# Performance work log

Hardware: AMD Instinct MI355X
Metric: run time of the kernel (lower is better)

Reference implementation:

```python
import jax, jax.numpy as jnp
import numpy as np

SRC_V, TRG_V = 36616, 23262
EMB, ENC_H, DEC_H = 300, 512, 1024
S, T, B = 50, 50, 128


def setup_inputs() -> dict:
    key = jax.random.key(0)
    ks = jax.random.split(key, 17)
    sc = 0.05
    n = lambda k, shp: (jax.random.normal(k, shp, jnp.float32) * sc)
    return {
        "input_src_batch": jax.random.randint(ks[0], (S, B), 0, SRC_V),
        "input_trg_batch": jax.random.randint(ks[1], (T, B), 0, TRG_V),
        "EEMB": n(ks[2], (SRC_V, EMB)),
        "enc_Wih_f": n(ks[3], (4 * ENC_H, EMB)),
        "enc_Whh_f": n(ks[4], (4 * ENC_H, ENC_H)),
        "enc_b_f": n(ks[5], (4 * ENC_H,)),
        "enc_Wih_r": n(ks[6], (4 * ENC_H, EMB)),
        "enc_Whh_r": n(ks[7], (4 * ENC_H, ENC_H)),
        "enc_b_r": n(ks[8], (4 * ENC_H,)),
        "attn_Wi": n(ks[9], (DEC_H, DEC_H)),
        "attn_Wo": n(ks[10], (DEC_H, 2 * DEC_H)),
        "dec_Wih": n(ks[11], (4 * DEC_H, DEC_H + EMB)),
        "dec_Whh": n(ks[12], (4 * DEC_H, DEC_H)),
        "dec_b": n(ks[13], (4 * DEC_H,)),
        "DEMB": n(ks[14], (TRG_V, EMB)),
        "gen_W": n(ks[15], (TRG_V, DEC_H)),
        "gen_b": n(ks[16], (TRG_V,)),
    }


def lstm_step(h, c, x, Wih, Whh, b):
    # PyTorch gate order: i, f, g, o
    g = x @ Wih.T + h @ Whh.T + b
    i, f, gg, o = jnp.split(g, 4, axis=-1)
    c2 = jax.nn.sigmoid(f) * c + jax.nn.sigmoid(i) * jnp.tanh(gg)
    h2 = jax.nn.sigmoid(o) * jnp.tanh(c2)
    return h2, c2


def reference(input_src_batch, input_trg_batch, EEMB, enc_Wih_f, enc_Whh_f,
              enc_b_f, enc_Wih_r, enc_Whh_r, enc_b_r, attn_Wi, attn_Wo,
              dec_Wih, dec_Whh, dec_b, DEMB, gen_W, gen_b):
    batch = input_src_batch.shape[1]
    sent_len = input_trg_batch.shape[0]
    emb = EEMB[input_src_batch]  # [S, B, 300]

    def scan_dir(xs, Wih, Whh, b):
        def f(carry, x):
            h, c = carry
            h2, c2 = lstm_step(h, c, x, Wih, Whh, b)
            return (h2, c2), h2
        init = (jnp.zeros((batch, ENC_H), emb.dtype),
                jnp.zeros((batch, ENC_H), emb.dtype))
        (hF, cF), hs = jax.lax.scan(f, init, xs)
        return hs, hF, cF

    hs_f, hF, cF = scan_dir(emb, enc_Wih_f, enc_Whh_f, enc_b_f)
    hs_r, hR, cR = scan_dir(emb[::-1], enc_Wih_r, enc_Whh_r, enc_b_r)
    hs_r = hs_r[::-1]
    enc_out = jnp.concatenate([hs_f, hs_r], axis=-1)  # [S, B, 1024]
    # torch permute(1,2,0).view(B,1024) interleaves fwd/rev per feature
    hidden = jnp.stack([hF, hR], axis=-1).reshape(batch, DEC_H)
    context = jnp.stack([cF, cR], axis=-1).reshape(batch, DEC_H)

    def attn(h):
        semi = h @ attn_Wi.T                                # [B,1024]
        score = jnp.einsum('sbd,bd->sb', enc_out, semi)     # [S,B]
        alpha = jax.nn.softmax(score, axis=0)               # softmax over src len
        s_tilde = jnp.einsum('sb,sbd->bd', alpha, enc_out)  # [B,1024]
        return jnp.tanh(jnp.concatenate([s_tilde, h], axis=1) @ attn_Wo.T)

    trg_emb = DEMB[input_trg_batch[: sent_len - 1]]  # [T-1, B, 300]

    def step(carry, x_emb):
        h, c = carry
        c_t = attn(h)
        dec_in = jnp.concatenate([c_t, x_emb], axis=1)  # [B, 1324]
        h2, c2 = lstm_step(h, c, dec_in, dec_Wih, dec_Whh, dec_b)
        logp = jax.nn.log_softmax(h2 @ gen_W.T + gen_b, axis=1)
        return (h2, c2), logp

    _, outs = jax.lax.scan(step, (hidden, context), trg_emb)  # [T-1,B,V]
    out0 = jnp.zeros((1, batch, TRG_V), outs.dtype)
    return jnp.concatenate([out0, outs], axis=0)  # [T, B, V]
```

## Files before the change

### kernel.cpp

```cpp
#include <hip/hip_runtime.h>
#include <hip/hip_bf16.h>

#define S_LEN 50
#define T_LEN 50
#define BATCH 128
#define EMB 300
#define ENC_H 512
#define DEC_H 1024
#define TRG_V 23262
#define DEC_IN (DEC_H + EMB)
#define KCAT (DEC_IN + DEC_H)

static inline int cdiv(int a, int b) { return (a + b - 1) / b; }

__device__ __forceinline__ float sigm(float x) { return 1.f / (1.f + expf(-x)); }

typedef __attribute__((ext_vector_type(8))) short bf16x8;
typedef __attribute__((ext_vector_type(4))) float f32x4;

__device__ __forceinline__ void gload_lds16(const void* g, void* l) {
    __builtin_amdgcn_global_load_lds((const __attribute__((address_space(1))) int*)g,
                                     (__attribute__((address_space(3))) int*)l, 16, 0, 0);
}

__global__ __launch_bounds__(256)
void gemm_mfma_bf16(const __hip_bfloat16* __restrict__ A, const __hip_bfloat16* __restrict__ W,
                    const float* __restrict__ bias, float* __restrict__ C,
                    int M, int N, int K, int ldc)
{
    __shared__ short As[128 * 32];
    __shared__ short Bs[128 * 32];
    const int tid  = threadIdx.x;
    const int wave = tid >> 6;
    const int lane = tid & 63;
    const int m0 = blockIdx.y * 128;
    const int n0 = blockIdx.x * 128;
    const int wr = wave >> 1, wc = wave & 1;

    const int srow = lane >> 2;
    const int kgrp = lane & 3;
    const int arow0 = 32 * wave;

    f32x4 acc[4][4] = {};

    for (int k0 = 0; k0 < K; k0 += 32) {
#pragma unroll
        for (int c = 0; c < 2; c++) {
            int row = arow0 + 16 * c + srow;
            gload_lds16(A + (size_t)(m0 + row) * K + k0 + kgrp * 8,
                        &As[(arow0 + 16 * c) * 32]);
        }
#pragma unroll
        for (int c = 0; c < 2; c++) {
            int row = arow0 + 16 * c + srow;
            int gr = n0 + row; if (gr > N - 1) gr = N - 1;
            gload_lds16(W + (size_t)gr * K + k0 + kgrp * 8,
                        &Bs[(arow0 + 16 * c) * 32]);
        }
        __syncthreads();

        bf16x8 a[4], b[4];
#pragma unroll
        for (int mi = 0; mi < 4; mi++)
            a[mi] = *(const bf16x8*)&As[(wr * 64 + mi * 16 + (lane & 15)) * 32 + (lane >> 4) * 8];
#pragma unroll
        for (int ni = 0; ni < 4; ni++)
            b[ni] = *(const bf16x8*)&Bs[(wc * 64 + ni * 16 + (lane & 15)) * 32 + (lane >> 4) * 8];
#pragma unroll
        for (int mi = 0; mi < 4; mi++)
#pragma unroll
            for (int ni = 0; ni < 4; ni++)
                acc[mi][ni] = __builtin_amdgcn_mfma_f32_16x16x32_bf16(a[mi], b[ni], acc[mi][ni], 0, 0, 0);
        __syncthreads();
    }

#pragma unroll
    for (int mi = 0; mi < 4; mi++)
#pragma unroll
        for (int ni = 0; ni < 4; ni++) {
            int col = n0 + wc * 64 + ni * 16 + (lane & 15);
            if (col >= N) continue;
            float bv = bias[col];
#pragma unroll
            for (int r = 0; r < 4; r++) {
                int row = m0 + wr * 64 + mi * 16 + (lane >> 4) * 4 + r;
                C[(size_t)row * ldc + col] = acc[mi][ni][r] + bv;
            }
        }
}

__global__ void cast_f32_bf16(const float* __restrict__ in, __hip_bfloat16* __restrict__ out, size_t n)
{
    size_t i = ((size_t)blockIdx.x * blockDim.x + threadIdx.x) * 4;
    if (i + 3 < n) {
        float4 v = *(const float4*)(in + i);
        out[i + 0] = __float2bfloat16(v.x);
        out[i + 1] = __float2bfloat16(v.y);
        out[i + 2] = __float2bfloat16(v.z);
        out[i + 3] = __float2bfloat16(v.w);
    } else {
        for (; i < n; i++) out[i] = __float2bfloat16(in[i]);
    }
}

template<int BM, int BN, int BK, int TM, int TN, bool HAS_BIAS>
__global__ __launch_bounds__((BM / TM) * (BN / TN))
void gemm_bt(const float* __restrict__ A, const float* __restrict__ W,
             const float* __restrict__ bias, float* __restrict__ C,
             int M, int N, int K, int ldc)
{
    constexpr int NT  = (BM / TM) * (BN / TN);
    constexpr int NGA = TM / 4;
    constexpr int NGB = TN / 4;
    constexpr int GS  = (BN / TN) * 4;
    constexpr int LPA = BM * BK / 4 / NT;
    constexpr int LPB = BN * BK / 4 / NT;

    __shared__ float As[BK][BM + 4];
    __shared__ float Bs[BK][BN + 4];

    const int tid = threadIdx.x;
    const int tx = tid % (BN / TN);
    const int ty = tid / (BN / TN);
    const int m0 = blockIdx.y * BM;
    const int n0 = blockIdx.x * BN;

    float acc[TM][TN];
#pragma unroll
    for (int i = 0; i < TM; i++)
#pragma unroll
        for (int j = 0; j < TN; j++) acc[i][j] = 0.f;

    for (int k0 = 0; k0 < K; k0 += BK) {
#pragma unroll
        for (int e = 0; e < LPA; e++) {
            int idx = tid + e * NT;
            int r = idx / (BK / 4);
            int c4 = idx % (BK / 4);
            int row = m0 + r; if (row > M - 1) row = M - 1;
            int kk = k0 + c4 * 4;
            float4 v;
            if (kk + 3 < K) {
                v = *(const float4*)(A + (size_t)row * K + kk);
            } else {
                v.x = (kk + 0 < K) ? A[(size_t)row * K + kk + 0] : 0.f;
                v.y = (kk + 1 < K) ? A[(size_t)row * K + kk + 1] : 0.f;
                v.z = (kk + 2 < K) ? A[(size_t)row * K + kk + 2] : 0.f;
                v.w = (kk + 3 < K) ? A[(size_t)row * K + kk + 3] : 0.f;
            }
            As[c4 * 4 + 0][r] = v.x; As[c4 * 4 + 1][r] = v.y;
            As[c4 * 4 + 2][r] = v.z; As[c4 * 4 + 3][r] = v.w;
        }
#pragma unroll
        for (int e = 0; e < LPB; e++) {
            int idx = tid + e * NT;
            int r = idx / (BK / 4);
            int c4 = idx % (BK / 4);
            int row = n0 + r; if (row > N - 1) row = N - 1;
            int kk = k0 + c4 * 4;
            float4 v;
            if (kk + 3 < K) {
                v = *(const float4*)(W + (size_t)row * K + kk);
            } else {
                v.x = (kk + 0 < K) ? W[(size_t)row * K + kk + 0] : 0.f;
                v.y = (kk + 1 < K) ? W[(size_t)row * K + kk + 1] : 0.f;
                v.z = (kk + 2 < K) ? W[(size_t)row * K + kk + 2] : 0.f;
                v.w = (kk + 3 < K) ? W[(size_t)row * K + kk + 3] : 0.f;
            }
            Bs[c4 * 4 + 0][r] = v.x; Bs[c4 * 4 + 1][r] = v.y;
            Bs[c4 * 4 + 2][r] = v.z; Bs[c4 * 4 + 3][r] = v.w;
        }
        __syncthreads();
#pragma unroll
        for (int kk = 0; kk < BK; kk++) {
            float a[TM], b[TN];
#pragma unroll
            for (int g = 0; g < NGA; g++) {
                float4 v = *(const float4*)(&As[kk][ty * TM + g * 4]);
                a[g * 4 + 0] = v.x; a[g * 4 + 1] = v.y; a[g * 4 + 2] = v.z; a[g * 4 + 3] = v.w;
            }
#pragma unroll
            for (int g = 0; g < NGB; g++) {
                float4 v = *(const float4*)(&Bs[kk][tx * 4 + g * GS]);
                b[g * 4 + 0] = v.x; b[g * 4 + 1] = v.y; b[g * 4 + 2] = v.z; b[g * 4 + 3] = v.w;
            }
#pragma unroll
            for (int i = 0; i < TM; i++)
#pragma unroll
                for (int j = 0; j < TN; j++)
                    acc[i][j] = fmaf(a[i], b[j], acc[i][j]);
        }
        __syncthreads();
    }

#pragma unroll
    for (int i = 0; i < TM; i++) {
        int row = m0 + ty * TM + i;
        if (row >= M) continue;
#pragma unroll
        for (int g = 0; g < NGB; g++) {
            int colb = n0 + tx * 4 + g * GS;
#pragma unroll
            for (int j = 0; j < 4; j++) {
                int cc = colb + j;
                if (cc >= N) continue;
                float v = acc[i][g * 4 + j];
                if (HAS_BIAS) v += bias[cc];
                C[(size_t)row * ldc + cc] = v;
            }
        }
    }
}

struct StepArgs {
    const float* bias;
    const float* D0; const float* D1;
    float* cst0; float* cst1;
    float* hst0; float* hst1;
    float* enc_out;
    float* catA;
    float* attn_cat;
    float* cdec;
    __hip_bfloat16* H_bf;
    int t;
};

__device__ __forceinline__ float4 g4k(const float* base, int kk, int K) {
    float4 v = make_float4(0.f, 0.f, 0.f, 0.f);
    if (kk + 3 < K) v = *(const float4*)(base + kk);
    else {
        if (kk     < K) v.x = base[kk];
        if (kk + 1 < K) v.y = base[kk + 1];
        if (kk + 2 < K) v.z = base[kk + 2];
    }
    return v;
}

template<int EPI, bool DUAL>
__global__ __launch_bounds__(256)
void step_gemm(const float* __restrict__ A, const float* __restrict__ W, int K,
               const float* __restrict__ A1, const float* __restrict__ W1,
               StepArgs ea)
{
    __shared__ float As[2][32][36];
    __shared__ float Bs[2][32][68];
    const int tid = threadIdx.x;
    const int tx = tid & 15, ty = tid >> 4;
    const int m0 = blockIdx.y * 32, n0 = blockIdx.x * 64;
    const int dir = DUAL ? blockIdx.z : 0;
    const float* Ap = (DUAL && dir) ? A1 : A;
    const float* Wp = (DUAL && dir) ? W1 : W;

    const int ar = tid >> 3, ac4 = tid & 7;
    const float* abase  = Ap + (size_t)(m0 + ar) * K;
    const float* bbase0 = Wp + (size_t)(n0 + ar) * K;
    const float* bbase1 = bbase0 + (size_t)32 * K;

    float acc[2][4] = {{0.f,0.f,0.f,0.f},{0.f,0.f,0.f,0.f}};
    const int NIT = (K + 31) / 32;

    float4 pa, pb0, pb1;
    {
        int kk = ac4 * 4;
        if (32 <= K) { pa = *(const float4*)(abase + kk); pb0 = *(const float4*)(bbase0 + kk); pb1 = *(const float4*)(bbase1 + kk); }
        else { pa = g4k(abase, kk, K); pb0 = g4k(bbase0, kk, K); pb1 = g4k(bbase1, kk, K); }
    }
    *(float4*)&As[0][ar][ac4 * 4] = pa;
    Bs[0][ac4*4+0][ar]    = pb0.x; Bs[0][ac4*4+1][ar]    = pb0.y;
    Bs[0][ac4*4+2][ar]    = pb0.z; Bs[0][ac4*4+3][ar]    = pb0.w;
    Bs[0][ac4*4+0][ar+32] = pb1.x; Bs[0][ac4*4+1][ar+32] = pb1.y;
    Bs[0][ac4*4+2][ar+32] = pb1.z; Bs[0][ac4*4+3][ar+32] = pb1.w;
    __syncthreads();

    int cur = 0;
    for (int it = 0; it < NIT; ++it) {
        float4 qa, qb0, qb1;
        const bool has = (it + 1 < NIT);
        if (has) {
            int k0 = (it + 1) * 32;
            int kk = k0 + ac4 * 4;
            if (k0 + 32 <= K) { qa = *(const float4*)(abase + kk); qb0 = *(const float4*)(bbase0 + kk); qb1 = *(const float4*)(bbase1 + kk); }
            else { qa = g4k(abase, kk, K); qb0 = g4k(bbase0, kk, K); qb1 = g4k(bbase1, kk, K); }
        }
#pragma unroll
        for (int k4 = 0; k4 < 8; ++k4) {
            float4 a0 = *(const float4*)&As[cur][ty*2+0][k4*4];
            float4 a1 = *(const float4*)&As[cur][ty*2+1][k4*4];
            float4 b0 = *(const float4*)&Bs[cur][k4*4+0][tx*4];
            float4 b1 = *(const float4*)&Bs[cur][k4*4+1][tx*4];
            float4 b2 = *(const float4*)&Bs[cur][k4*4+2][tx*4];
            float4 b3 = *(const float4*)&Bs[cur][k4*4+3][tx*4];
            float av0[4] = {a0.x, a0.y, a0.z, a0.w};
            float av1[4] = {a1.x, a1.y, a1.z, a1.w};
            float4 bq[4] = {b0, b1, b2, b3};
#pragma unroll
            for (int q = 0; q < 4; q++) {
                acc[0][0] = fmaf(av0[q], bq[q].x, acc[0][0]);
                acc[0][1] = fmaf(av0[q], bq[q].y, acc[0][1]);
                acc[0][2] = fmaf(av0[q], bq[q].z, acc[0][2]);
                acc[0][3] = fmaf(av0[q], bq[q].w, acc[0][3]);
                acc[1][0] = fmaf(av1[q], bq[q].x, acc[1][0]);
                acc[1][1] = fmaf(av1[q], bq[q].y, acc[1][1]);
                acc[1][2] = fmaf(av1[q], bq[q].z, acc[1][2]);
                acc[1][3] = fmaf(av1[q], bq[q].w, acc[1][3]);
            }
        }
        if (has) {
            int nb = cur ^ 1;
            *(float4*)&As[nb][ar][ac4 * 4] = qa;
            Bs[nb][ac4*4+0][ar]    = qb0.x; Bs[nb][ac4*4+1][ar]    = qb0.y;
            Bs[nb][ac4*4+2][ar]    = qb0.z; Bs[nb][ac4*4+3][ar]    = qb0.w;
            Bs[nb][ac4*4+0][ar+32] = qb1.x; Bs[nb][ac4*4+1][ar+32] = qb1.y;
            Bs[nb][ac4*4+2][ar+32] = qb1.z; Bs[nb][ac4*4+3][ar+32] = qb1.w;
        }
        __syncthreads();
        cur ^= 1;
    }

    const int cb = n0 + tx * 4;
    if (EPI == 1) {
#pragma unroll
        for (int i = 0; i < 2; i++) {
            int row = m0 + ty * 2 + i;
            float* dst = ea.catA + (size_t)row * KCAT + cb;
            dst[0] = tanhf(acc[i][0]); dst[1] = tanhf(acc[i][1]);
            dst[2] = tanhf(acc[i][2]); dst[3] = tanhf(acc[i][3]);
        }
    } else if (EPI == 2) {
        const float* D = dir ? ea.D1 : ea.D0;
        float* cst = dir ? ea.cst1 : ea.cst0;
        float* hst = dir ? ea.hst1 : ea.hst0;
        int j = cb >> 2;
        int s_out = dir ? (S_LEN - 1 - ea.t) : ea.t;
#pragma unroll
        for (int i = 0; i < 2; i++) {
            int b = m0 + ty * 2 + i;
            float4 d = *(const float4*)(D + (size_t)b * (4 * ENC_H) + cb);
            float gi = acc[i][0] + d.x, gf = acc[i][1] + d.y;
            float gg = acc[i][2] + d.z, go = acc[i][3] + d.w;
            float c2 = sigm(gf) * cst[b * ENC_H + j] + sigm(gi) * tanhf(gg);
            float h2 = sigm(go) * tanhf(c2);
            cst[b * ENC_H + j] = c2;
            hst[b * ENC_H + j] = h2;
            ea.enc_out[((size_t)s_out * BATCH + b) * DEC_H + dir * ENC_H + j] = h2;
        }
    } else if (EPI == 3) {
        int j = cb >> 2;
        float4 bz = *(const float4*)(ea.bias + cb);
#pragma unroll
        for (int i = 0; i < 2; i++) {
            int b = m0 + ty * 2 + i;
            float gi = acc[i][0] + bz.x, gf = acc[i][1] + bz.y;
            float gg = acc[i][2] + bz.z, go = acc[i][3] + bz.w;
            float c2 = sigm(gf) * ea.cdec[b * DEC_H + j] + sigm(gi) * tanhf(gg);
            float h2 = sigm(go) * tanhf(c2);
            ea.cdec[b * DEC_H + j] = c2;
            ea.H_bf[(size_t)ea.t * BATCH * DEC_H + b * DEC_H + j] = __float2bfloat16(h2);
            ea.attn_cat[(size_t)b * 2 * DEC_H + DEC_H + j] = h2;
        }
    }
}

__global__ void zero_f32(float* p, size_t n) {
    size_t i = (size_t)blockIdx.x * blockDim.x + threadIdx.x;
    if (i < n) p[i] = 0.f;
}

__global__ void gather_rows(const int* __restrict__ ids, const float* __restrict__ E,
                            float* __restrict__ out, int nrows, int width)
{
    size_t i = (size_t)blockIdx.x * blockDim.x + threadIdx.x;
    size_t total = (size_t)nrows * width;
    if (i >= total) return;
    int r = (int)(i / width);
    int e = (int)(i % width);
    out[i] = E[(size_t)ids[r] * width + e];
}

__global__ void interleave_rows(const float* __restrict__ src, float* __restrict__ dst,
                                int units, int kdim)
{
    size_t i = (size_t)blockIdx.x * blockDim.x + threadIdx.x;
    size_t total = (size_t)4 * units * kdim;
    if (i >= total) return;
    int ir = (int)(i / kdim), k = (int)(i % kdim);
    int gate = ir & 3, j = ir >> 2;
    dst[i] = src[(size_t)(gate * units + j) * kdim + k];
}

__global__ void interleave_vec(const float* __restrict__ src, float* __restrict__ dst, int units)
{
    int i = blockIdx.x * blockDim.x + threadIdx.x;
    if (i >= 4 * units) return;
    int gate = i & 3, j = i >> 2;
    dst[i] = src[gate * units + j];
}

__global__ void build_wcat_int(const float* __restrict__ Wih, const float* __restrict__ Whh,
                               float* __restrict__ dst)
{
    size_t i = (size_t)blockIdx.x * blockDim.x + threadIdx.x;
    if (i >= (size_t)4 * DEC_H * KCAT) return;
    int ir = (int)(i / KCAT), k = (int)(i % KCAT);
    int gate = ir & 3, j = ir >> 2;
    int r = gate * DEC_H + j;
    dst[i] = (k < DEC_IN) ? Wih[(size_t)r * DEC_IN + k] : Whh[(size_t)r * DEC_H + (k - DEC_IN)];
}

__global__ void transpose_sq(const float* __restrict__ src, float* __restrict__ dst, int n)
{
    int i = blockIdx.x * blockDim.x + threadIdx.x;
    if (i >= n * n) return;
    int r = i / n, c = i % n;
    dst[(size_t)r * n + c] = src[(size_t)c * n + r];
}

__global__ void dec_init2(const float* __restrict__ hF, const float* __restrict__ cF,
                          const float* __restrict__ hR, const float* __restrict__ cR,
                          float* __restrict__ attn_cat, float* __restrict__ cdec)
{
    int idx = blockIdx.x * blockDim.x + threadIdx.x;
    if (idx >= BATCH * DEC_H) return;
    int b = idx / DEC_H, j = idx % DEC_H;
    int half = j >> 1;
    float h = (j & 1) ? hR[b * ENC_H + half] : hF[b * ENC_H + half];
    float c = (j & 1) ? cR[b * ENC_H + half] : cF[b * ENC_H + half];
    attn_cat[(size_t)b * 2 * DEC_H + DEC_H + j] = h;
    cdec[idx] = c;
}

__global__ __launch_bounds__(256)
void attn_fused(const float* __restrict__ encP, const float* __restrict__ enc_out,
                const float* __restrict__ trg_emb, float* __restrict__ attn_cat,
                float* __restrict__ catA, int t)
{
    int b = blockIdx.x, tid = threadIdx.x;
    __shared__ float hv[DEC_H];
    __shared__ float sc[S_LEN];
    for (int d = tid; d < DEC_H; d += 256) hv[d] = attn_cat[(size_t)b * 2 * DEC_H + DEC_H + d];
    __syncthreads();
    for (int e = tid; e < EMB; e += 256)
        catA[(size_t)b * KCAT + DEC_H + e] = trg_emb[((size_t)t * BATCH + b) * EMB + e];
    for (int d = tid; d < DEC_H; d += 256)
        catA[(size_t)b * KCAT + DEC_IN + d] = hv[d];
    int wave = tid >> 6, lane = tid & 63;
    for (int s = wave; s < S_LEN; s += 4) {
        const float* e = encP + ((size_t)s * BATCH + b) * DEC_H;
        float p = 0.f;
        for (int d = lane; d < DEC_H; d += 64) p = fmaf(e[d], hv[d], p);
        for (int off = 32; off; off >>= 1) p += __shfl_down(p, off);
        if (lane == 0) sc[s] = p;
    }
    __syncthreads();
    if (tid < 64) {
        float x = (tid < S_LEN) ? sc[tid] : -1e30f;
        float m = x;
        for (int off = 32; off; off >>= 1) m = fmaxf(m, __shfl_xor(m, off));
        float ex = (tid < S_LEN) ? expf(x - m) : 0.f;
        float ssum = ex;
        for (int off = 32; off; off >>= 1) ssum += __shfl_xor(ssum, off);
        if (tid < S_LEN) sc[tid] = ex / ssum;
    }
    __syncthreads();
    for (int d = tid; d < DEC_H; d += 256) {
        float a = 0.f;
#pragma unroll 5
        for (int s = 0; s < S_LEN; s++)
            a = fmaf(sc[s], enc_out[((size_t)s * BATCH + b) * DEC_H + d], a);
        attn_cat[(size_t)b * 2 * DEC_H + d] = a;
    }
}

__global__ __launch_bounds__(256)
void log_softmax_rows(float* __restrict__ X, int V)
{
    int row = blockIdx.x;
    float* x = X + (size_t)row * V;
    int tid = threadIdx.x;
    __shared__ float redm[4], reds[4];
    float m = -1e30f;
    for (int i = tid; i < V; i += 256) m = fmaxf(m, x[i]);
    for (int off = 32; off; off >>= 1) m = fmaxf(m, __shfl_xor(m, off));
    if ((tid & 63) == 0) redm[tid >> 6] = m;
    __syncthreads();
    m = fmaxf(fmaxf(redm[0], redm[1]), fmaxf(redm[2], redm[3]));
    float s = 0.f;
    for (int i = tid; i < V; i += 256) s += expf(x[i] - m);
    for (int off = 32; off; off >>= 1) s += __shfl_xor(s, off);
    if ((tid & 63) == 0) reds[tid >> 6] = s;
    __syncthreads();
    s = reds[0] + reds[1] + reds[2] + reds[3];
    float lg = m + logf(s);
    for (int i = tid; i < V; i += 256) x[i] -= lg;
}

static void launch_gemm_big_bias(const float* A, const float* W, const float* bias, float* C,
                                 int M, int N, int K, int ldc, hipStream_t s)
{
    dim3 g(cdiv(N, 128), cdiv(M, 128), 1);
    gemm_bt<128, 128, 16, 8, 8, true><<<g, 256, 0, s>>>(A, W, bias, C, M, N, K, ldc);
}
static void launch_gemm_big(const float* A, const float* W, float* C,
                            int M, int N, int K, int ldc, hipStream_t s)
{
    dim3 g(cdiv(N, 128), cdiv(M, 128), 1);
    gemm_bt<128, 128, 16, 8, 8, false><<<g, 256, 0, s>>>(A, W, nullptr, C, M, N, K, ldc);
}

extern "C" void kernel_launch(void* const* d_in, const int* in_sizes, int n_in,
                              void* d_out, int out_size, void* d_ws, size_t ws_size,
                              hipStream_t stream)
{
    const int*   src   = (const int*)d_in[0];
    const int*   trg   = (const int*)d_in[1];
    const float* EEMBp = (const float*)d_in[2];
    const float* eWihF = (const float*)d_in[3];
    const float* eWhhF = (const float*)d_in[4];
    const float* ebF   = (const float*)d_in[5];
    const float* eWihR = (const float*)d_in[6];
    const float* eWhhR = (const float*)d_in[7];
    const float* ebR   = (const float*)d_in[8];
    const float* aWi   = (const float*)d_in[9];
    const float* aWo   = (const float*)d_in[10];
    const float* dWih  = (const float*)d_in[11];
    const float* dWhh  = (const float*)d_in[12];
    const float* db    = (const float*)d_in[13];
    const float* DEMBp = (const float*)d_in[14];
    const float* gW    = (const float*)d_in[15];
    const float* gb    = (const float*)d_in[16];
    float* out = (float*)d_out;
    float* ws  = (float*)d_ws;

    size_t off = 0;
    auto alloc = [&](size_t n) { float* p = ws + off; off += n; return p; };

    float* Gf      = alloc((size_t)S_LEN * BATCH * 4 * ENC_H);
    float* Gr      = alloc((size_t)S_LEN * BATCH * 4 * ENC_H);
    float* emb_src = alloc((size_t)S_LEN * BATCH * EMB);
    float* enc_out = alloc((size_t)S_LEN * BATCH * DEC_H);
    float* hF2     = alloc((size_t)2 * BATCH * ENC_H);
    float* hR2     = alloc((size_t)2 * BATCH * ENC_H);
    float* cF      = alloc(BATCH * ENC_H);
    float* cR      = alloc(BATCH * ENC_H);
    float* trg_emb = alloc((size_t)(T_LEN - 1) * BATCH * EMB);
    float* wihF_i  = alloc((size_t)4 * ENC_H * EMB);
    float* wihR_i  = alloc((size_t)4 * ENC_H * EMB);
    float* whhF_i  = alloc((size_t)4 * ENC_H * ENC_H);
    float* whhR_i  = alloc((size_t)4 * ENC_H * ENC_H);
    float* ebF_i   = alloc(4 * ENC_H);
    float* ebR_i   = alloc(4 * ENC_H);
    float* wcat_i  = alloc((size_t)4 * DEC_H * KCAT);
    float* db_i    = alloc(4 * DEC_H);
    float* aWiT    = alloc((size_t)DEC_H * DEC_H);
    float* cdec    = alloc(BATCH * DEC_H);
    float* attn_cat= alloc((size_t)BATCH * 2 * DEC_H);
    float* catA    = alloc((size_t)BATCH * KCAT);
    __hip_bfloat16* H_bf = (__hip_bfloat16*)alloc((size_t)(T_LEN - 1) * BATCH * DEC_H / 2);
    __hip_bfloat16* gWb  = (__hip_bfloat16*)Gf;
    float* encP = Gr;

    const int HS = BATCH * ENC_H;

    zero_f32<<<cdiv(BATCH * TRG_V, 256), 256, 0, stream>>>(out, (size_t)BATCH * TRG_V);
    zero_f32<<<cdiv(6 * HS, 256), 256, 0, stream>>>(hF2, (size_t)6 * HS);

    gather_rows<<<cdiv(S_LEN * BATCH * EMB, 256), 256, 0, stream>>>(src, EEMBp, emb_src, S_LEN * BATCH, EMB);
    gather_rows<<<cdiv((T_LEN - 1) * BATCH * EMB, 256), 256, 0, stream>>>(trg, DEMBp, trg_emb, (T_LEN - 1) * BATCH, EMB);

    interleave_rows<<<cdiv(4 * ENC_H * EMB, 256), 256, 0, stream>>>(eWihF, wihF_i, ENC_H, EMB);
    interleave_rows<<<cdiv(4 * ENC_H * EMB, 256), 256, 0, stream>>>(eWihR, wihR_i, ENC_H, EMB);
    interleave_rows<<<cdiv(4 * ENC_H * ENC_H, 256), 256, 0, stream>>>(eWhhF, whhF_i, ENC_H, ENC_H);
    interleave_rows<<<cdiv(4 * ENC_H * ENC_H, 256), 256, 0, stream>>>(eWhhR, whhR_i, ENC_H, ENC_H);
    interleave_vec<<<cdiv(4 * ENC_H, 256), 256, 0, stream>>>(ebF, ebF_i, ENC_H);
    interleave_vec<<<cdiv(4 * ENC_H, 256), 256, 0, stream>>>(ebR, ebR_i, ENC_H);
    build_wcat_int<<<cdiv(4 * DEC_H * KCAT, 256), 256, 0, stream>>>(dWih, dWhh, wcat_i);
    interleave_vec<<<cdiv(4 * DEC_H, 256), 256, 0, stream>>>(db, db_i, DEC_H);
    transpose_sq<<<cdiv(DEC_H * DEC_H, 256), 256, 0, stream>>>(aWi, aWiT, DEC_H);

    launch_gemm_big_bias(emb_src, wihF_i, ebF_i, Gf, S_LEN * BATCH, 4 * ENC_H, EMB, 4 * ENC_H, stream);
    launch_gemm_big_bias(emb_src, wihR_i, ebR_i, Gr, S_LEN * BATCH, 4 * ENC_H, EMB, 4 * ENC_H, stream);

    for (int t = 0; t < S_LEN; t++) {
        StepArgs ea{};
        ea.D0 = Gf + (size_t)t * BATCH * 4 * ENC_H;
        ea.D1 = Gr + (size_t)(S_LEN - 1 - t) * BATCH * 4 * ENC_H;
        ea.cst0 = cF; ea.cst1 = cR;
        ea.hst0 = hF2 + ((t + 1) & 1) * HS;
        ea.hst1 = hR2 + ((t + 1) & 1) * HS;
        ea.enc_out = enc_out; ea.t = t;
        dim3 g(4 * ENC_H / 64, BATCH / 32, 2);
        step_gemm<2, true><<<g, 256, 0, stream>>>(hF2 + (t & 1) * HS, whhF_i, ENC_H,
                                                  hR2 + (t & 1) * HS, whhR_i, ea);
    }

    launch_gemm_big(enc_out, aWiT, encP, S_LEN * BATCH, DEC_H, DEC_H, DEC_H, stream);

    cast_f32_bf16<<<cdiv((int)((size_t)TRG_V * DEC_H / 4), 256), 256, 0, stream>>>(gW, gWb, (size_t)TRG_V * DEC_H);

    dec_init2<<<cdiv(BATCH * DEC_H, 256), 256, 0, stream>>>(hF2, cF, hR2, cR, attn_cat, cdec);

    for (int t = 0; t < T_LEN - 1; t++) {
        attn_fused<<<BATCH, 256, 0, stream>>>(encP, enc_out, trg_emb, attn_cat, catA, t);
        {
            StepArgs ea{}; ea.catA = catA;
            dim3 g(DEC_H / 64, BATCH / 32, 1);
            step_gemm<1, false><<<g, 256, 0, stream>>>(attn_cat, aWo, 2 * DEC_H, nullptr, nullptr, ea);
        }
        {
            StepArgs ea{};
            ea.bias = db_i; ea.cdec = cdec; ea.attn_cat = attn_cat; ea.H_bf = H_bf; ea.t = t;
            dim3 g(4 * DEC_H / 64, BATCH / 32, 1);
            step_gemm<3, false><<<g, 256, 0, stream>>>(catA, wcat_i, KCAT, nullptr, nullptr, ea);
        }
    }

    {
        dim3 g(cdiv(TRG_V, 128), cdiv((T_LEN - 1) * BATCH, 128), 1);
        gemm_mfma_bf16<<<g, 256, 0, stream>>>(H_bf, gWb, gb, out + (size_t)BATCH * TRG_V,
                                              (T_LEN - 1) * BATCH, TRG_V, DEC_H, TRG_V);
    }

    log_softmax_rows<<<(T_LEN - 1) * BATCH, 256, 0, stream>>>(out + (size_t)BATCH * TRG_V, TRG_V);
}
```

Before: 12.18 ms.

## Replace per-step encoder/decoder kernel launches with persistent kernels using grid barriers

The encoder recurrence and the decoder loop now each run inside one persistent 256-block kernel, with an atomic-counter global barrier between dependent phases instead of a separate launch per step. The decoder also splits the attn_Wo GEMM so the h-half runs concurrently with attention, and it gathers target embeddings inline instead of in a separate pass. This removes roughly 200 kernel launches and their gaps. In exchange it depends on all 256 blocks being co-resident, since the spin barrier can deadlock otherwise, and it pays atomic spin costs at every barrier.

```diff
diff --git a/kernel.cpp b/kernel.cpp
--- a/kernel.cpp
+++ b/kernel.cpp
@@ -21,6 +21,18 @@
 __device__ __forceinline__ void gload_lds16(const void* g, void* l) {
     __builtin_amdgcn_global_load_lds((const __attribute__((address_space(1))) int*)g,
                                      (__attribute__((address_space(3))) int*)l, 16, 0, 0);
+}
+
+__device__ __forceinline__ void gbar(unsigned* cnt, unsigned target) {
+    __syncthreads();
+    if (threadIdx.x == 0) {
+        __threadfence();
+        atomicAdd(cnt, 1u);
+        while (__hip_atomic_load(cnt, __ATOMIC_ACQUIRE, __HIP_MEMORY_SCOPE_AGENT) < target)
+            __builtin_amdgcn_s_sleep(2);
+        __threadfence();
+    }
+    __syncthreads();
 }
 
 __global__ __launch_bounds__(256)
@@ -212,19 +224,6 @@
     }
 }
 
-struct StepArgs {
-    const float* bias;
-    const float* D0; const float* D1;
-    float* cst0; float* cst1;
-    float* hst0; float* hst1;
-    float* enc_out;
-    float* catA;
-    float* attn_cat;
-    float* cdec;
-    __hip_bfloat16* H_bf;
-    int t;
-};
-
 __device__ __forceinline__ float4 g4k(const float* base, int kk, int K) {
     float4 v = make_float4(0.f, 0.f, 0.f, 0.f);
     if (kk + 3 < K) v = *(const float4*)(base + kk);
@@ -236,40 +235,34 @@
     return v;
 }
 
-template<int EPI, bool DUAL>
-__global__ __launch_bounds__(256)
-void step_gemm(const float* __restrict__ A, const float* __restrict__ W, int K,
-               const float* __restrict__ A1, const float* __restrict__ W1,
-               StepArgs ea)
-{
-    __shared__ float As[2][32][36];
-    __shared__ float Bs[2][32][68];
+__device__ __forceinline__ void tile_core(
+    float (&As)[2][32][36], float (&Bs)[2][32][68],
+    const float* __restrict__ A, int lda,
+    const float* __restrict__ W, int ldw, int K,
+    int m0, int n0, float (&acc)[2][4])
+{
     const int tid = threadIdx.x;
     const int tx = tid & 15, ty = tid >> 4;
-    const int m0 = blockIdx.y * 32, n0 = blockIdx.x * 64;
-    const int dir = DUAL ? blockIdx.z : 0;
-    const float* Ap = (DUAL && dir) ? A1 : A;
-    const float* Wp = (DUAL && dir) ? W1 : W;
-
     const int ar = tid >> 3, ac4 = tid & 7;
-    const float* abase  = Ap + (size_t)(m0 + ar) * K;
-    const float* bbase0 = Wp + (size_t)(n0 + ar) * K;
-    const float* bbase1 = bbase0 + (size_t)32 * K;
-
-    float acc[2][4] = {{0.f,0.f,0.f,0.f},{0.f,0.f,0.f,0.f}};
+    const float* abase = A + (size_t)(m0 + ar) * lda;
+    const float* bb0   = W + (size_t)(n0 + ar) * ldw;
+    const float* bb1   = bb0 + (size_t)32 * ldw;
+
+    acc[0][0]=acc[0][1]=acc[0][2]=acc[0][3]=0.f;
+    acc[1][0]=acc[1][1]=acc[1][2]=acc[1][3]=0.f;
     const int NIT = (K + 31) / 32;
 
-    float4 pa, pb0, pb1;
     {
         int kk = ac4 * 4;
-        if (32 <= K) { pa = *(const float4*)(abase + kk); pb0 = *(const float4*)(bbase0 + kk); pb1 = *(const float4*)(bbase1 + kk); }
-        else { pa = g4k(abase, kk, K); pb0 = g4k(bbase0, kk, K); pb1 = g4k(bbase1, kk, K); }
-    }
-    *(float4*)&As[0][ar][ac4 * 4] = pa;
-    Bs[0][ac4*4+0][ar]    = pb0.x; Bs[0][ac4*4+1][ar]    = pb0.y;
-    Bs[0][ac4*4+2][ar]    = pb0.z; Bs[0][ac4*4+3][ar]    = pb0.w;
-    Bs[0][ac4*4+0][ar+32] = pb1.x; Bs[0][ac4*4+1][ar+32] = pb1.y;
-    Bs[0][ac4*4+2][ar+32] = pb1.z; Bs[0][ac4*4+3][ar+32] = pb1.w;
+        float4 pa  = *(const float4*)(abase + kk);
+        float4 pb0 = *(const float4*)(bb0 + kk);
+        float4 pb1 = *(const float4*)(bb1 + kk);
+        *(float4*)&As[0][ar][ac4 * 4] = pa;
+        Bs[0][ac4*4+0][ar]    = pb0.x; Bs[0][ac4*4+1][ar]    = pb0.y;
+        Bs[0][ac4*4+2][ar]    = pb0.z; Bs[0][ac4*4+3][ar]    = pb0.w;
+        Bs[0][ac4*4+0][ar+32] = pb1.x; Bs[0][ac4*4+1][ar+32] = pb1.y;
+        Bs[0][ac4*4+2][ar+32] = pb1.z; Bs[0][ac4*4+3][ar+32] = pb1.w;
+    }
     __syncthreads();
 
     int cur = 0;
@@ -279,8 +272,8 @@
         if (has) {
             int k0 = (it + 1) * 32;
             int kk = k0 + ac4 * 4;
-            if (k0 + 32 <= K) { qa = *(const float4*)(abase + kk); qb0 = *(const float4*)(bbase0 + kk); qb1 = *(const float4*)(bbase1 + kk); }
-            else { qa = g4k(abase, kk, K); qb0 = g4k(bbase0, kk, K); qb1 = g4k(bbase1, kk, K); }
+            if (k0 + 32 <= K) { qa = *(const float4*)(abase + kk); qb0 = *(const float4*)(bb0 + kk); qb1 = *(const float4*)(bb1 + kk); }
+            else { qa = g4k(abase, kk, K); qb0 = g4k(bb0, kk, K); qb1 = g4k(bb1, kk, K); }
         }
 #pragma unroll
         for (int k4 = 0; k4 < 8; ++k4) {
@@ -316,48 +309,170 @@
         __syncthreads();
         cur ^= 1;
     }
-
-    const int cb = n0 + tx * 4;
-    if (EPI == 1) {
-#pragma unroll
-        for (int i = 0; i < 2; i++) {
-            int row = m0 + ty * 2 + i;
-            float* dst = ea.catA + (size_t)row * KCAT + cb;
-            dst[0] = tanhf(acc[i][0]); dst[1] = tanhf(acc[i][1]);
-            dst[2] = tanhf(acc[i][2]); dst[3] = tanhf(acc[i][3]);
-        }
-    } else if (EPI == 2) {
-        const float* D = dir ? ea.D1 : ea.D0;
-        float* cst = dir ? ea.cst1 : ea.cst0;
-        float* hst = dir ? ea.hst1 : ea.hst0;
-        int j = cb >> 2;
-        int s_out = dir ? (S_LEN - 1 - ea.t) : ea.t;
+}
+
+__device__ __forceinline__ void attn_body(
+    int b, int t, float* hv, float* sc,
+    const float* __restrict__ encP, const float* __restrict__ enc_out,
+    const int* __restrict__ trg, const float* __restrict__ DEMB,
+    float* __restrict__ attn_cat, float* __restrict__ catA)
+{
+    const int tid = threadIdx.x;
+    for (int d = tid; d < DEC_H; d += 256) {
+        float h = attn_cat[(size_t)b * 2 * DEC_H + DEC_H + d];
+        hv[d] = h;
+        catA[(size_t)b * KCAT + DEC_IN + d] = h;
+    }
+    int id0 = trg[t * BATCH + b];
+    for (int e = tid; e < EMB; e += 256)
+        catA[(size_t)b * KCAT + DEC_H + e] = DEMB[(size_t)id0 * EMB + e];
+    __syncthreads();
+    int wave = tid >> 6, lane = tid & 63;
+    for (int s = wave; s < S_LEN; s += 4) {
+        const float* e = encP + ((size_t)s * BATCH + b) * DEC_H;
+        float p = 0.f;
+        for (int d = lane; d < DEC_H; d += 64) p = fmaf(e[d], hv[d], p);
+        for (int off = 32; off; off >>= 1) p += __shfl_down(p, off);
+        if (lane == 0) sc[s] = p;
+    }
+    __syncthreads();
+    if (tid < 64) {
+        float x = (tid < S_LEN) ? sc[tid] : -1e30f;
+        float m = x;
+        for (int off = 32; off; off >>= 1) m = fmaxf(m, __shfl_xor(m, off));
+        float ex = (tid < S_LEN) ? expf(x - m) : 0.f;
+        float ssum = ex;
+        for (int off = 32; off; off >>= 1) ssum += __shfl_xor(ssum, off);
+        if (tid < S_LEN) sc[tid] = ex / ssum;
+    }
+    __syncthreads();
+    for (int d = tid; d < DEC_H; d += 256) {
+        float a = 0.f;
+#pragma unroll 5
+        for (int s = 0; s < S_LEN; s++)
+            a = fmaf(sc[s], enc_out[((size_t)s * BATCH + b) * DEC_H + d], a);
+        attn_cat[(size_t)b * 2 * DEC_H + d] = a;
+    }
+}
+
+__global__ __launch_bounds__(256)
+void enc_persistent(const float* __restrict__ Gf, const float* __restrict__ Gr,
+                    const float* __restrict__ whhF, const float* __restrict__ whhR,
+                    float* __restrict__ hF2, float* __restrict__ hR2,
+                    float* __restrict__ cF, float* __restrict__ cR,
+                    float* __restrict__ enc_out, unsigned* __restrict__ barcnt)
+{
+    __shared__ struct { float As[2][32][36]; float Bs[2][32][68]; } sm;
+    const int blk = blockIdx.x;
+    const int tid = threadIdx.x;
+    const int tx = tid & 15, ty = tid >> 4;
+    const int dir = blk >> 7;
+    const int id  = blk & 127;
+    const int m0 = (id >> 5) * 32;
+    const int n0 = (id & 31) * 64;
+    const float* W  = dir ? whhR : whhF;
+    float* cst      = dir ? cR : cF;
+    float* hbase    = dir ? hR2 : hF2;
+    const float* G  = dir ? Gr : Gf;
+    const int HS = BATCH * ENC_H;
+    unsigned epoch = 0;
+    float acc[2][4];
+
+    for (int t = 0; t < S_LEN; ++t) {
+        const float* h_in = hbase + (size_t)(t & 1) * HS;
+        float* h_out      = hbase + (size_t)((t + 1) & 1) * HS;
+        int s_g = dir ? (S_LEN - 1 - t) : t;
+        const float* D = G + (size_t)s_g * BATCH * 4 * ENC_H;
+
+        tile_core(sm.As, sm.Bs, h_in, ENC_H, W, ENC_H, ENC_H, m0, n0, acc);
+
+        int cb = n0 + tx * 4, j = cb >> 2;
 #pragma unroll
         for (int i = 0; i < 2; i++) {
             int b = m0 + ty * 2 + i;
-            float4 d = *(const float4*)(D + (size_t)b * (4 * ENC_H) + cb);
-            float gi = acc[i][0] + d.x, gf = acc[i][1] + d.y;
-            float gg = acc[i][2] + d.z, go = acc[i][3] + d.w;
+            float4 d4 = *(const float4*)(D + (size_t)b * 4 * ENC_H + cb);
+            float gi = acc[i][0] + d4.x, gf = acc[i][1] + d4.y;
+            float gg = acc[i][2] + d4.z, go = acc[i][3] + d4.w;
             float c2 = sigm(gf) * cst[b * ENC_H + j] + sigm(gi) * tanhf(gg);
             float h2 = sigm(go) * tanhf(c2);
             cst[b * ENC_H + j] = c2;
-            hst[b * ENC_H + j] = h2;
-            ea.enc_out[((size_t)s_out * BATCH + b) * DEC_H + dir * ENC_H + j] = h2;
-        }
-    } else if (EPI == 3) {
-        int j = cb >> 2;
-        float4 bz = *(const float4*)(ea.bias + cb);
-#pragma unroll
-        for (int i = 0; i < 2; i++) {
-            int b = m0 + ty * 2 + i;
-            float gi = acc[i][0] + bz.x, gf = acc[i][1] + bz.y;
-            float gg = acc[i][2] + bz.z, go = acc[i][3] + bz.w;
-            float c2 = sigm(gf) * ea.cdec[b * DEC_H + j] + sigm(gi) * tanhf(gg);
-            float h2 = sigm(go) * tanhf(c2);
-            ea.cdec[b * DEC_H + j] = c2;
-            ea.H_bf[(size_t)ea.t * BATCH * DEC_H + b * DEC_H + j] = __float2bfloat16(h2);
-            ea.attn_cat[(size_t)b * 2 * DEC_H + DEC_H + j] = h2;
-        }
+            h_out[b * ENC_H + j] = h2;
+            enc_out[((size_t)s_g * BATCH + b) * DEC_H + dir * ENC_H + j] = h2;
+        }
+        if (t < S_LEN - 1) gbar(barcnt, 256u * (++epoch));
+    }
+}
+
+__global__ __launch_bounds__(256)
+void dec_persistent(const float* __restrict__ encP, const float* __restrict__ enc_out,
+                    const int* __restrict__ trg, const float* __restrict__ DEMB,
+                    const float* __restrict__ aWo, const float* __restrict__ wcat,
+                    const float* __restrict__ db_i,
+                    float* __restrict__ attn_cat, float* __restrict__ catA,
+                    float* __restrict__ cdec, __hip_bfloat16* __restrict__ H_bf,
+                    unsigned* __restrict__ barcnt)
+{
+    __shared__ union {
+        struct { float hv[DEC_H]; float sc[S_LEN]; } a;
+        struct { float As[2][32][36]; float Bs[2][32][68]; } g;
+    } sm;
+    const int blk = blockIdx.x;
+    const int tid = threadIdx.x;
+    const int tx = tid & 15, ty = tid >> 4;
+    unsigned epoch = 0;
+    float acc[2][4];
+
+    for (int t = 0; t < T_LEN - 1; ++t) {
+        if (blk < 128) {
+            attn_body(blk, t, sm.a.hv, sm.a.sc, encP, enc_out, trg, DEMB, attn_cat, catA);
+        } else if (blk < 192) {
+            int id = blk - 128;
+            int m0 = (id >> 4) * 32, n0 = (id & 15) * 64;
+            tile_core(sm.g.As, sm.g.Bs, attn_cat + DEC_H, 2 * DEC_H,
+                      aWo + DEC_H, 2 * DEC_H, DEC_H, m0, n0, acc);
+            int cb = n0 + tx * 4;
+#pragma unroll
+            for (int i = 0; i < 2; i++) {
+                int row = m0 + ty * 2 + i;
+                float* dst = catA + (size_t)row * KCAT + cb;
+                dst[0] = acc[i][0]; dst[1] = acc[i][1];
+                dst[2] = acc[i][2]; dst[3] = acc[i][3];
+            }
+        }
+        gbar(barcnt, 256u * (++epoch));
+
+        if (blk < 64) {
+            int m0 = (blk >> 4) * 32, n0 = (blk & 15) * 64;
+            tile_core(sm.g.As, sm.g.Bs, attn_cat, 2 * DEC_H, aWo, 2 * DEC_H, DEC_H, m0, n0, acc);
+            int cb = n0 + tx * 4;
+#pragma unroll
+            for (int i = 0; i < 2; i++) {
+                int row = m0 + ty * 2 + i;
+                float* dst = catA + (size_t)row * KCAT + cb;
+                dst[0] = tanhf(acc[i][0] + dst[0]); dst[1] = tanhf(acc[i][1] + dst[1]);
+                dst[2] = tanhf(acc[i][2] + dst[2]); dst[3] = tanhf(acc[i][3] + dst[3]);
+            }
+        }
+        gbar(barcnt, 256u * (++epoch));
+
+        {
+            int m0 = (blk >> 6) * 32, n0 = (blk & 63) * 64;
+            tile_core(sm.g.As, sm.g.Bs, catA, KCAT, wcat, KCAT, KCAT, m0, n0, acc);
+            int cb = n0 + tx * 4, j = cb >> 2;
+            float4 bz = *(const float4*)(db_i + cb);
+#pragma unroll
+            for (int i = 0; i < 2; i++) {
+                int b = m0 + ty * 2 + i;
+                float gi = acc[i][0] + bz.x, gf = acc[i][1] + bz.y;
+                float gg = acc[i][2] + bz.z, go = acc[i][3] + bz.w;
+                float c2 = sigm(gf) * cdec[b * DEC_H + j] + sigm(gi) * tanhf(gg);
+                float h2 = sigm(go) * tanhf(c2);
+                cdec[b * DEC_H + j] = c2;
+                H_bf[(size_t)t * BATCH * DEC_H + b * DEC_H + j] = __float2bfloat16(h2);
+                attn_cat[(size_t)b * 2 * DEC_H + DEC_H + j] = h2;
+            }
+        }
+        if (t < T_LEN - 2) gbar(barcnt, 256u * (++epoch));
     }
 }
 
@@ -427,48 +542,6 @@
     float c = (j & 1) ? cR[b * ENC_H + half] : cF[b * ENC_H + half];
     attn_cat[(size_t)b * 2 * DEC_H + DEC_H + j] = h;
     cdec[idx] = c;
-}
-
-__global__ __launch_bounds__(256)
-void attn_fused(const float* __restrict__ encP, const float* __restrict__ enc_out,
-                const float* __restrict__ trg_emb, float* __restrict__ attn_cat,
-                float* __restrict__ catA, int t)
-{
-    int b = blockIdx.x, tid = threadIdx.x;
-    __shared__ float hv[DEC_H];
-    __shared__ float sc[S_LEN];
-    for (int d = tid; d < DEC_H; d += 256) hv[d] = attn_cat[(size_t)b * 2 * DEC_H + DEC_H + d];
-    __syncthreads();
-    for (int e = tid; e < EMB; e += 256)
-        catA[(size_t)b * KCAT + DEC_H + e] = trg_emb[((size_t)t * BATCH + b) * EMB + e];
-    for (int d = tid; d < DEC_H; d += 256)
-        catA[(size_t)b * KCAT + DEC_IN + d] = hv[d];
-    int wave = tid >> 6, lane = tid & 63;
-    for (int s = wave; s < S_LEN; s += 4) {
-        const float* e = encP + ((size_t)s * BATCH + b) * DEC_H;
-        float p = 0.f;
-        for (int d = lane; d < DEC_H; d += 64) p = fmaf(e[d], hv[d], p);
-        for (int off = 32; off; off >>= 1) p += __shfl_down(p, off);
-        if (lane == 0) sc[s] = p;
-    }
-    __syncthreads();
-    if (tid < 64) {
-        float x = (tid < S_LEN) ? sc[tid] : -1e30f;
-        float m = x;
-        for (int off = 32; off; off >>= 1) m = fmaxf(m, __shfl_xor(m, off));
-        float ex = (tid < S_LEN) ? expf(x - m) : 0.f;
-        float ssum = ex;
-        for (int off = 32; off; off >>= 1) ssum += __shfl_xor(ssum, off);
-        if (tid < S_LEN) sc[tid] = ex / ssum;
-    }
-    __syncthreads();
-    for (int d = tid; d < DEC_H; d += 256) {
-        float a = 0.f;
-#pragma unroll 5
-        for (int s = 0; s < S_LEN; s++)
-            a = fmaf(sc[s], enc_out[((size_t)s * BATCH + b) * DEC_H + d], a);
-        attn_cat[(size_t)b * 2 * DEC_H + d] = a;
-    }
 }
 
 __global__ __launch_bounds__(256)
@@ -542,7 +615,6 @@
     float* hR2     = alloc((size_t)2 * BATCH * ENC_H);
     float* cF      = alloc(BATCH * ENC_H);
     float* cR      = alloc(BATCH * ENC_H);
-    float* trg_emb = alloc((size_t)(T_LEN - 1) * BATCH * EMB);
     float* wihF_i  = alloc((size_t)4 * ENC_H * EMB);
     float* wihR_i  = alloc((size_t)4 * ENC_H * EMB);
     float* whhF_i  = alloc((size_t)4 * ENC_H * ENC_H);
@@ -556,16 +628,17 @@
     float* attn_cat= alloc((size_t)BATCH * 2 * DEC_H);
     float* catA    = alloc((size_t)BATCH * KCAT);
     __hip_bfloat16* H_bf = (__hip_bfloat16*)alloc((size_t)(T_LEN - 1) * BATCH * DEC_H / 2);
-    __hip_bfloat16* gWb  = (__hip_bfloat16*)Gf;
+    unsigned* barcnt = (unsigned*)alloc(16);
+    __hip_bfloat16* gWb = (__hip_bfloat16*)Gf;
     float* encP = Gr;
 
     const int HS = BATCH * ENC_H;
 
     zero_f32<<<cdiv(BATCH * TRG_V, 256), 256, 0, stream>>>(out, (size_t)BATCH * TRG_V);
     zero_f32<<<cdiv(6 * HS, 256), 256, 0, stream>>>(hF2, (size_t)6 * HS);
+    zero_f32<<<1, 16, 0, stream>>>((float*)barcnt, 16);
 
     gather_rows<<<cdiv(S_LEN * BATCH * EMB, 256), 256, 0, stream>>>(src, EEMBp, emb_src, S_LEN * BATCH, EMB);
-    gather_rows<<<cdiv((T_LEN - 1) * BATCH * EMB, 256), 256, 0, stream>>>(trg, DEMBp, trg_emb, (T_LEN - 1) * BATCH, EMB);
 
     interleave_rows<<<cdiv(4 * ENC_H * EMB, 256), 256, 0, stream>>>(eWihF, wihF_i, ENC_H, EMB);
     interleave_rows<<<cdiv(4 * ENC_H * EMB, 256), 256, 0, stream>>>(eWihR, wihR_i, ENC_H, EMB);
@@ -580,18 +653,8 @@
     launch_gemm_big_bias(emb_src, wihF_i, ebF_i, Gf, S_LEN * BATCH, 4 * ENC_H, EMB, 4 * ENC_H, stream);
     launch_gemm_big_bias(emb_src, wihR_i, ebR_i, Gr, S_LEN * BATCH, 4 * ENC_H, EMB, 4 * ENC_H, stream);
 
-    for (int t = 0; t < S_LEN; t++) {
-        StepArgs ea{};
-        ea.D0 = Gf + (size_t)t * BATCH * 4 * ENC_H;
-        ea.D1 = Gr + (size_t)(S_LEN - 1 - t) * BATCH * 4 * ENC_H;
-        ea.cst0 = cF; ea.cst1 = cR;
-        ea.hst0 = hF2 + ((t + 1) & 1) * HS;
-        ea.hst1 = hR2 + ((t + 1) & 1) * HS;
-        ea.enc_out = enc_out; ea.t = t;
-        dim3 g(4 * ENC_H / 64, BATCH / 32, 2);
-        step_gemm<2, true><<<g, 256, 0, stream>>>(hF2 + (t & 1) * HS, whhF_i, ENC_H,
-                                                  hR2 + (t & 1) * HS, whhR_i, ea);
-    }
+    enc_persistent<<<256, 256, 0, stream>>>(Gf, Gr, whhF_i, whhR_i, hF2, hR2, cF, cR,
+                                            enc_out, &barcnt[0]);
 
     launch_gemm_big(enc_out, aWiT, encP, S_LEN * BATCH, DEC_H, DEC_H, DEC_H, stream);
 
@@ -599,20 +662,8 @@
 
     dec_init2<<<cdiv(BATCH * DEC_H, 256), 256, 0, stream>>>(hF2, cF, hR2, cR, attn_cat, cdec);
 
-    for (int t = 0; t < T_LEN - 1; t++) {
-        attn_fused<<<BATCH, 256, 0, stream>>>(encP, enc_out, trg_emb, attn_cat, catA, t);
-        {
-            StepArgs ea{}; ea.catA = catA;
-            dim3 g(DEC_H / 64, BATCH / 32, 1);
-            step_gemm<1, false><<<g, 256, 0, stream>>>(attn_cat, aWo, 2 * DEC_H, nullptr, nullptr, ea);
-        }
-        {
-            StepArgs ea{};
-            ea.bias = db_i; ea.cdec = cdec; ea.attn_cat = attn_cat; ea.H_bf = H_bf; ea.t = t;
-            dim3 g(4 * DEC_H / 64, BATCH / 32, 1);
-            step_gemm<3, false><<<g, 256, 0, stream>>>(catA, wcat_i, KCAT, nullptr, nullptr, ea);
-        }
-    }
+    dec_persistent<<<256, 256, 0, stream>>>(encP, enc_out, trg, DEMBp, aWo, wcat_i, db_i,
+                                            attn_cat, catA, cdec, H_bf, &barcnt[1]);
 
     {
         dim3 g(cdiv(TRG_V, 128), cdiv((T_LEN - 1) * BATCH, 128), 1);
```

Result: slower. 25.17 ms (+106.7%).
